# Performance work log

Hardware: AMD Instinct MI355X
Metric: run time of the kernel (lower is better)

## Reference

```python
import jax, jax.numpy as jnp
import numpy as np

B, S, ENC = 64, 60, 1024
E, H, V, T = 512, 512, 32000, 20


def setup_inputs() -> dict:
    key = jax.random.key(0)
    ks = jax.random.split(key, 10)
    sc = lambda n: 1.0 / np.sqrt(n)
    return {
        "encoder_outputs": jax.random.normal(ks[0], (B, S, ENC), jnp.float32),
        "captions": jax.random.randint(ks[1], (B, T), 0, V, jnp.int64),
        "emb_table": jax.random.normal(ks[2], (V, E), jnp.float32) * 0.02,
        "attn_W": jax.random.uniform(ks[3], (H, ENC), jnp.float32, -sc(ENC), sc(ENC)),
        "attn_b": jnp.zeros((H,), jnp.float32),
        "W_ih": jax.random.uniform(ks[4], (4 * H, E + ENC), jnp.float32, -sc(H), sc(H)),
        "W_hh": jax.random.uniform(ks[5], (4 * H, H), jnp.float32, -sc(H), sc(H)),
        "b_ih": jnp.zeros((4 * H,), jnp.float32),
        "b_hh": jnp.zeros((4 * H,), jnp.float32),
        "fc_W": jax.random.uniform(ks[6], (V, H), jnp.float32, -sc(H), sc(H)),
        "fc_b": jnp.zeros((V,), jnp.float32),
    }


def reference(encoder_outputs, captions, emb_table, attn_W, attn_b,
              W_ih, W_hh, b_ih, b_hh, fc_W, fc_b):
    # Luong attention key projection is h-independent: hoist out of the loop.
    proj = jnp.einsum('bse,he->bsh', encoder_outputs, attn_W) + attn_b  # [B,S,H]

    def step(carry, prev_word):
        h, c = carry
        emb = emb_table[prev_word]                                  # [B,E]
        scores = jnp.einsum('bsh,bh->bs', proj, h)                  # [B,S]
        w = jax.nn.softmax(scores, axis=1)
        ctx = jnp.einsum('bs,bse->be', w, encoder_outputs)          # [B,ENC]
        x = jnp.concatenate([emb, ctx], axis=1)                     # [B,E+ENC]
        gates = x @ W_ih.T + b_ih + h @ W_hh.T + b_hh               # [B,4H]
        i, f, g, o = jnp.split(gates, 4, axis=1)
        c2 = jax.nn.sigmoid(f) * c + jax.nn.sigmoid(i) * jnp.tanh(g)
        h2 = jax.nn.sigmoid(o) * jnp.tanh(c2)
        out = h2 @ fc_W.T + fc_b                                    # [B,V] (dropout = eval identity)
        return (h2, c2), (out, w)

    h0 = jnp.zeros((B, H), encoder_outputs.dtype)
    c0 = jnp.zeros((B, H), encoder_outputs.dtype)
    prev_words = captions[:, :-1].T                                 # teacher forcing: [T-1,B]
    _, (outs, attns) = jax.lax.scan(step, (h0, c0), prev_words)
    outputs = jnp.concatenate(
        [jnp.zeros((B, 1, V), outs.dtype), outs.transpose(1, 0, 2)], axis=1)  # [B,T,V]
    return outputs, attns
```

## Files before the change

### kernel.cpp

```cpp
#include <hip/hip_runtime.h>
#include <math.h>
#include <stdint.h>

#define BB   64
#define SS   60
#define ENCD 1024
#define ED   512
#define HD   512
#define VD   32000
#define TT   20

typedef unsigned short u16;
typedef __attribute__((ext_vector_type(8))) short short8v;
typedef __attribute__((ext_vector_type(4))) float f32x4;

__device__ __forceinline__ u16 f2bf(float x) {
  unsigned int u = __float_as_uint(x);
  return (u16)((u + 0x7FFFu + ((u >> 16) & 1u)) >> 16);
}
__device__ __forceinline__ float bf2f(u16 b) {
  return __uint_as_float((unsigned)b << 16);
}

__global__ __launch_bounds__(256) void init_kernel(float* __restrict__ out,
                                                   float* __restrict__ h,
                                                   float* __restrict__ c) {
  int i = blockIdx.x * 256 + threadIdx.x;
  if (i < BB * VD) {
    int b = i / VD, v = i - b * VD;
    out[(long)b * (TT * VD) + v] = 0.f;
  }
  if (i < BB * HD) { h[i] = 0.f; c[i] = 0.f; }
}

__global__ __launch_bounds__(256) void convert_bf16_k(const float* __restrict__ src,
                                                      u16* __restrict__ dst, long n) {
  long i = ((long)blockIdx.x * 256 + threadIdx.x) * 8;
  if (i + 8 <= n) {
    float4 a = *reinterpret_cast<const float4*>(src + i);
    float4 b = *reinterpret_cast<const float4*>(src + i + 4);
    uint4 o;
    o.x = (unsigned)f2bf(a.x) | ((unsigned)f2bf(a.y) << 16);
    o.y = (unsigned)f2bf(a.z) | ((unsigned)f2bf(a.w) << 16);
    o.z = (unsigned)f2bf(b.x) | ((unsigned)f2bf(b.y) << 16);
    o.w = (unsigned)f2bf(b.z) | ((unsigned)f2bf(b.w) << 16);
    *reinterpret_cast<uint4*>(dst + i) = o;
  }
}

__global__ __launch_bounds__(256) void split_pair_k(const float* __restrict__ src,
                                                    u16* __restrict__ bf,
                                                    u16* __restrict__ er, long n) {
  long i = ((long)blockIdx.x * 256 + threadIdx.x) * 8;
  if (i + 8 <= n) {
    #pragma unroll
    for (int j = 0; j < 8; ++j) {
      float v = src[i + j];
      u16 b = f2bf(v);
      bf[i + j] = b;
      er[i + j] = f2bf(v - bf2f(b));
    }
  }
}

__global__ __launch_bounds__(256) void split_wg_k(
    const float* __restrict__ Wih, const float* __restrict__ Whh,
    u16* __restrict__ wb, u16* __restrict__ we) {
  int n = blockIdx.x;
  int k0 = threadIdx.x * 8;
  #pragma unroll
  for (int j = 0; j < 8; ++j) {
    int k = k0 + j;
    float v = (k < 1536) ? Wih[(long)n * 1536 + k] : Whh[(long)n * 512 + (k - 1536)];
    u16 b = f2bf(v);
    wb[(long)n * 2048 + k] = b;
    we[(long)n * 2048 + k] = f2bf(v - bf2f(b));
  }
}

__global__ __launch_bounds__(256) void gather_emb_split(
    const int* __restrict__ caps, const float* __restrict__ emb,
    u16* __restrict__ xb, u16* __restrict__ xe) {
  int r = blockIdx.x;
  int b = r & 63, t = r >> 6;
  int word = caps[b * TT + t];
  const float* src = emb + (long)word * ED;
  for (int k = threadIdx.x; k < ED; k += 256) {
    float v = src[k];
    u16 bb = f2bf(v);
    xb[(long)r * ED + k] = bb;
    xe[(long)r * ED + k] = f2bf(v - bf2f(bb));
  }
}

__global__ __launch_bounds__(256) void gates_mfma(
    const u16* __restrict__ xb, const u16* __restrict__ xe,
    const u16* __restrict__ wb, const u16* __restrict__ we,
    float* __restrict__ P) {
  __shared__ __align__(16) u16 lds[32768];
  const int tid = threadIdx.x;
  const int n0 = blockIdx.x * 64;
  const int kz = blockIdx.z * 256;
  const int w = tid >> 6, lane = tid & 63;
  const int frow = lane & 15, fgrp = lane >> 4;
  const int srow = tid >> 3, sslot = tid & 7;
  const int scol = (sslot ^ (srow & 7)) * 8;
  char* L = (char*)lds;

#define GT_STAGE(buf, kc) do {                                                     \
    _Pragma("unroll")                                                              \
    for (int ii = 0; ii < 2; ++ii) {                                               \
      int r_ = ii * 32 + srow;                                                     \
      __builtin_amdgcn_global_load_lds(                                            \
        (const __attribute__((address_space(1))) void*)(xb + (long)r_ * 2048 + (kc) + scol), \
        (__attribute__((address_space(3))) void*)(L + (buf) * 8192 + ii * 4096 + tid * 16), 16, 0, 0); \
      __builtin_amdgcn_global_load_lds(                                            \
        (const __attribute__((address_space(1))) void*)(xe + (long)r_ * 2048 + (kc) + scol), \
        (__attribute__((address_space(3))) void*)(L + 16384 + (buf) * 8192 + ii * 4096 + tid * 16), 16, 0, 0); \
      __builtin_amdgcn_global_load_lds(                                            \
        (const __attribute__((address_space(1))) void*)(wb + (long)(n0 + r_) * 2048 + (kc) + scol), \
        (__attribute__((address_space(3))) void*)(L + 32768 + (buf) * 8192 + ii * 4096 + tid * 16), 16, 0, 0); \
      __builtin_amdgcn_global_load_lds(                                            \
        (const __attribute__((address_space(1))) void*)(we + (long)(n0 + r_) * 2048 + (kc) + scol), \
        (__attribute__((address_space(3))) void*)(L + 49152 + (buf) * 8192 + ii * 4096 + tid * 16), 16, 0, 0); \
    }                                                                              \
  } while (0)

  f32x4 acc[4] = {{0.f,0.f,0.f,0.f},{0.f,0.f,0.f,0.f},{0.f,0.f,0.f,0.f},{0.f,0.f,0.f,0.f}};

  GT_STAGE(0, kz);
  asm volatile("s_waitcnt vmcnt(0)");
  __syncthreads();

  for (int kc = 0; kc < 4; ++kc) {
    const int cur = kc & 1;
    if (kc < 3) GT_STAGE(cur ^ 1, kz + (kc + 1) * 64);
    const char* Ab = L + cur * 8192;
    const char* Ae = L + 16384 + cur * 8192;
    const char* Bb = L + 32768 + cur * 8192;
    const char* Be = L + 49152 + cur * 8192;
    #pragma unroll
    for (int ks = 0; ks < 2; ++ks) {
      const int slot = ((ks * 4 + fgrp) ^ (frow & 7)) * 16;
      const int brow = (w * 16 + frow) * 128 + slot;
      short8v bbf = *reinterpret_cast<const short8v*>(Bb + brow);
      short8v bef = *reinterpret_cast<const short8v*>(Be + brow);
      #pragma unroll
      for (int m = 0; m < 4; ++m) {
        const int arow = (m * 16 + frow) * 128 + slot;
        short8v abf = *reinterpret_cast<const short8v*>(Ab + arow);
        short8v aef = *reinterpret_cast<const short8v*>(Ae + arow);
        acc[m] = __builtin_amdgcn_mfma_f32_16x16x32_bf16(abf, bbf, acc[m], 0, 0, 0);
        acc[m] = __builtin_amdgcn_mfma_f32_16x16x32_bf16(aef, bbf, acc[m], 0, 0, 0);
        acc[m] = __builtin_amdgcn_mfma_f32_16x16x32_bf16(abf, bef, acc[m], 0, 0, 0);
      }
    }
    asm volatile("s_waitcnt vmcnt(0)");
    __syncthreads();
  }

  float* Pz = P + (long)blockIdx.z * (BB * 2048);
  const int col = n0 + w * 16 + frow;
  #pragma unroll
  for (int m = 0; m < 4; ++m)
    #pragma unroll
    for (int r = 0; r < 4; ++r)
      Pz[(long)(m * 16 + fgrp * 4 + r) * 2048 + col] = acc[m][r];
#undef GT_STAGE
}

__global__ __launch_bounds__(256) void pemb_mfma(
    const u16* __restrict__ xb, const u16* __restrict__ xe,
    const u16* __restrict__ wb, const u16* __restrict__ we,
    float* __restrict__ Pemb) {
  __shared__ __align__(16) u16 lds[32768];
  const int tid = threadIdx.x;
  const int n0 = blockIdx.x * 64;
  const int t  = blockIdx.y;
  const u16* Ab_g = xb + (long)t * 64 * ED;
  const u16* Ae_g = xe + (long)t * 64 * ED;
  const int w = tid >> 6, lane = tid & 63;
  const int frow = lane & 15, fgrp = lane >> 4;
  const int srow = tid >> 3, sslot = tid & 7;
  const int scol = (sslot ^ (srow & 7)) * 8;
  char* L = (char*)lds;

#define PE_STAGE(buf, kc) do {                                                     \
    _Pragma("unroll")                                                              \
    for (int ii = 0; ii < 2; ++ii) {                                               \
      int r_ = ii * 32 + srow;                                                     \
      __builtin_amdgcn_global_load_lds(                                            \
        (const __attribute__((address_space(1))) void*)(Ab_g + (long)r_ * ED + (kc) + scol), \
        (__attribute__((address_space(3))) void*)(L + (buf) * 8192 + ii * 4096 + tid * 16), 16, 0, 0); \
      __builtin_amdgcn_global_load_lds(                                            \
        (const __attribute__((address_space(1))) void*)(Ae_g + (long)r_ * ED + (kc) + scol), \
        (__attribute__((address_space(3))) void*)(L + 16384 + (buf) * 8192 + ii * 4096 + tid * 16), 16, 0, 0); \
      __builtin_amdgcn_global_load_lds(                                            \
        (const __attribute__((address_space(1))) void*)(wb + (long)(n0 + r_) * 2048 + (kc) + scol), \
        (__attribute__((address_space(3))) void*)(L + 32768 + (buf) * 8192 + ii * 4096 + tid * 16), 16, 0, 0); \
      __builtin_amdgcn_global_load_lds(                                            \
        (const __attribute__((address_space(1))) void*)(we + (long)(n0 + r_) * 2048 + (kc) + scol), \
        (__attribute__((address_space(3))) void*)(L + 49152 + (buf) * 8192 + ii * 4096 + tid * 16), 16, 0, 0); \
    }                                                                              \
  } while (0)

  f32x4 acc[4] = {{0.f,0.f,0.f,0.f},{0.f,0.f,0.f,0.f},{0.f,0.f,0.f,0.f},{0.f,0.f,0.f,0.f}};

  PE_STAGE(0, 0);
  asm volatile("s_waitcnt vmcnt(0)");
  __syncthreads();

  for (int kc = 0; kc < 8; ++kc) {
    const int cur = kc & 1;
    if (kc < 7) PE_STAGE(cur ^ 1, (kc + 1) * 64);
    const char* Ab = L + cur * 8192;
    const char* Ae = L + 16384 + cur * 8192;
    const char* Bb = L + 32768 + cur * 8192;
    const char* Be = L + 49152 + cur * 8192;
    #pragma unroll
    for (int ks = 0; ks < 2; ++ks) {
      const int slot = ((ks * 4 + fgrp) ^ (frow & 7)) * 16;
      const int brow = (w * 16 + frow) * 128 + slot;
      short8v bbf = *reinterpret_cast<const short8v*>(Bb + brow);
      short8v bef = *reinterpret_cast<const short8v*>(Be + brow);
      #pragma unroll
      for (int m = 0; m < 4; ++m) {
        const int arow = (m * 16 + frow) * 128 + slot;
        short8v abf = *reinterpret_cast<const short8v*>(Ab + arow);
        short8v aef = *reinterpret_cast<const short8v*>(Ae + arow);
        acc[m] = __builtin_amdgcn_mfma_f32_16x16x32_bf16(abf, bbf, acc[m], 0, 0, 0);
        acc[m] = __builtin_amdgcn_mfma_f32_16x16x32_bf16(aef, bbf, acc[m], 0, 0, 0);
        acc[m] = __builtin_amdgcn_mfma_f32_16x16x32_bf16(abf, bef, acc[m], 0, 0, 0);
      }
    }
    asm volatile("s_waitcnt vmcnt(0)");
    __syncthreads();
  }

  float* Pz = Pemb + (long)t * (BB * 2048);
  const int col = n0 + w * 16 + frow;
  #pragma unroll
  for (int m = 0; m < 4; ++m)
    #pragma unroll
    for (int r = 0; r < 4; ++r)
      Pz[(long)(m * 16 + fgrp * 4 + r) * 2048 + col] = acc[m][r];
#undef PE_STAGE
}

__global__ __launch_bounds__(256) void proj_mfma(
    const u16* __restrict__ eb, const u16* __restrict__ ee,
    const u16* __restrict__ wb, const u16* __restrict__ we,
    const float* __restrict__ bias,
    float* __restrict__ proj) {
  __shared__ __align__(16) u16 lds[32768];
  const int tid = threadIdx.x;
  const int n0 = blockIdx.x * 64;
  const int m0 = blockIdx.y * 64;
  const int w = tid >> 6, lane = tid & 63;
  const int frow = lane & 15, fgrp = lane >> 4;
  const int srow = tid >> 3, sslot = tid & 7;
  const int scol = (sslot ^ (srow & 7)) * 8;
  char* L = (char*)lds;

#define PJ_STAGE(buf, kc) do {                                                     \
    _Pragma("unroll")                                                              \
    for (int ii = 0; ii < 2; ++ii) {                                               \
      int r_ = ii * 32 + srow;                                                     \
      __builtin_amdgcn_global_load_lds(                                            \
        (const __attribute__((address_space(1))) void*)(eb + (long)(m0 + r_) * ENCD + (kc) + scol), \
        (__attribute__((address_space(3))) void*)(L + (buf) * 8192 + ii * 4096 + tid * 16), 16, 0, 0); \
      __builtin_amdgcn_global_load_lds(                                            \
        (const __attribute__((address_space(1))) void*)(ee + (long)(m0 + r_) * ENCD + (kc) + scol), \
        (__attribute__((address_space(3))) void*)(L + 16384 + (buf) * 8192 + ii * 4096 + tid * 16), 16, 0, 0); \
      __builtin_amdgcn_global_load_lds(                                            \
        (const __attribute__((address_space(1))) void*)(wb + (long)(n0 + r_) * ENCD + (kc) + scol), \
        (__attribute__((address_space(3))) void*)(L + 32768 + (buf) * 8192 + ii * 4096 + tid * 16), 16, 0, 0); \
      __builtin_amdgcn_global_load_lds(                                            \
        (const __attribute__((address_space(1))) void*)(we + (long)(n0 + r_) * ENCD + (kc) + scol), \
        (__attribute__((address_space(3))) void*)(L + 49152 + (buf) * 8192 + ii * 4096 + tid * 16), 16, 0, 0); \
    }                                                                              \
  } while (0)

  f32x4 acc[4] = {{0.f,0.f,0.f,0.f},{0.f,0.f,0.f,0.f},{0.f,0.f,0.f,0.f},{0.f,0.f,0.f,0.f}};

  PJ_STAGE(0, 0);
  asm volatile("s_waitcnt vmcnt(0)");
  __syncthreads();

  for (int kc = 0; kc < 16; ++kc) {
    const int cur = kc & 1;
    if (kc < 15) PJ_STAGE(cur ^ 1, (kc + 1) * 64);
    const char* Ab = L + cur * 8192;
    const char* Ae = L + 16384 + cur * 8192;
    const char* Bb = L + 32768 + cur * 8192;
    const char* Be = L + 49152 + cur * 8192;
    #pragma unroll
    for (int ks = 0; ks < 2; ++ks) {
      const int slot = ((ks * 4 + fgrp) ^ (frow & 7)) * 16;
      const int brow = (w * 16 + frow) * 128 + slot;
      short8v bbf = *reinterpret_cast<const short8v*>(Bb + brow);
      short8v bef = *reinterpret_cast<const short8v*>(Be + brow);
      #pragma unroll
      for (int m = 0; m < 4; ++m) {
        const int arow = (m * 16 + frow) * 128 + slot;
        short8v abf = *reinterpret_cast<const short8v*>(Ab + arow);
        short8v aef = *reinterpret_cast<const short8v*>(Ae + arow);
        acc[m] = __builtin_amdgcn_mfma_f32_16x16x32_bf16(abf, bbf, acc[m], 0, 0, 0);
        acc[m] = __builtin_amdgcn_mfma_f32_16x16x32_bf16(aef, bbf, acc[m], 0, 0, 0);
        acc[m] = __builtin_amdgcn_mfma_f32_16x16x32_bf16(abf, bef, acc[m], 0, 0, 0);
      }
    }
    asm volatile("s_waitcnt vmcnt(0)");
    __syncthreads();
  }

  const int col = n0 + w * 16 + frow;
  const float bv = bias[col];
  #pragma unroll
  for (int m = 0; m < 4; ++m)
    #pragma unroll
    for (int r = 0; r < 4; ++r)
      proj[(long)(m0 + m * 16 + fgrp * 4 + r) * HD + col] = acc[m][r] + bv;
#undef PJ_STAGE
}

__global__ __launch_bounds__(256) void fc_tiled(
    const u16* __restrict__ hbuf, const u16* __restrict__ Wb,
    const float* __restrict__ bias, float* __restrict__ out) {
  __shared__ __align__(16) u16 lds[40960];
  const int tid = threadIdx.x;
  const int bid = blockIdx.x;
  const int xcd = bid & 7, loc = bid >> 3;
  const int wg = (xcd < 7) ? (xcd * 297 + loc) : (2079 + loc);
  const int n_tile = wg / 19, t = wg - n_tile * 19;
  const int n0 = n_tile * 256;

  const u16* Ab = hbuf + (long)t * (BB * HD);
  const u16* Wbase = Wb + (long)n0 * HD;

  const int w = tid >> 6, lane = tid & 63;
  const int frow = lane & 15, fgrp = lane >> 4;
  const int srow = tid >> 3, sslot = tid & 7;
  const int scol = (sslot ^ (srow & 7)) * 8;
  char* ldsb = (char*)lds;

#define FC_STAGE(buf, kc) do {                                                    \
    _Pragma("unroll")                                                             \
    for (int ii = 0; ii < 2; ++ii) {                                              \
      __builtin_amdgcn_global_load_lds(                                           \
        (const __attribute__((address_space(1))) void*)(Ab + (ii * 32 + srow) * HD + (kc) + scol), \
        (__attribute__((address_space(3))) void*)(ldsb + (buf) * 8192 + ii * 4096 + tid * 16), \
        16, 0, 0);                                                                \
    }                                                                             \
    _Pragma("unroll")                                                             \
    for (int ii = 0; ii < 8; ++ii) {                                              \
      __builtin_amdgcn_global_load_lds(                                           \
        (const __attribute__((address_space(1))) void*)(Wbase + (long)(ii * 32 + srow) * HD + (kc) + scol), \
        (__attribute__((address_space(3))) void*)(ldsb + 16384 + (buf) * 32768 + ii * 4096 + tid * 16), \
        16, 0, 0);                                                                \
    }                                                                             \
  } while (0)

  f32x4 acc[4][4] = {};

  FC_STAGE(0, 0);
  asm volatile("s_waitcnt vmcnt(0)");
  __syncthreads();

  for (int kc = 0; kc < 8; ++kc) {
    const int cur = kc & 1;
    if (kc < 7) FC_STAGE(cur ^ 1, (kc + 1) * 64);
    const char* Abuf = ldsb + cur * 8192;
    const char* Wbuf = ldsb + 16384 + cur * 32768;
    #pragma unroll
    for (int ks = 0; ks < 2; ++ks) {
      const int slot = ((ks * 4 + fgrp) ^ (frow & 7)) * 16;
      short8v af[4], wf[4];
      #pragma unroll
      for (int m = 0; m < 4; ++m)
        af[m] = *reinterpret_cast<const short8v*>(Abuf + (m * 16 + frow) * 128 + slot);
      #pragma unroll
      for (int n = 0; n < 4; ++n)
        wf[n] = *reinterpret_cast<const short8v*>(Wbuf + (w * 64 + n * 16 + frow) * 128 + slot);
      #pragma unroll
      for (int m = 0; m < 4; ++m)
        #pragma unroll
        for (int n = 0; n < 4; ++n)
          acc[m][n] = __builtin_amdgcn_mfma_f32_16x16x32_bf16(af[m], wf[n], acc[m][n], 0, 0, 0);
    }
    asm volatile("s_waitcnt vmcnt(0)");
    __syncthreads();
  }

  float* Lt = (float*)lds;
  #pragma unroll
  for (int n = 0; n < 4; ++n)
    #pragma unroll
    for (int m = 0; m < 4; ++m)
      #pragma unroll
      for (int r = 0; r < 4; ++r)
        Lt[(m * 16 + fgrp * 4 + r) * 260 + w * 64 + n * 16 + frow] = acc[m][n][r];
  __syncthreads();
  float4 bv4 = *reinterpret_cast<const float4*>(bias + n0 + lane * 4);
  #pragma unroll
  for (int i = 0; i < 16; ++i) {
    int row = w * 16 + i;
    float4 v = *reinterpret_cast<const float4*>(&Lt[row * 260 + lane * 4]);
    v.x += bv4.x; v.y += bv4.y; v.z += bv4.z; v.w += bv4.w;
    *reinterpret_cast<float4*>(out + ((long)row * TT + (t + 1)) * VD + n0 + lane * 4) = v;
  }
#undef FC_STAGE
}

__global__ __launch_bounds__(512) void fused_attn_lstm2(
    const float* __restrict__ proj, const float* __restrict__ enc,
    int t,
    const float* __restrict__ P,
    const float* __restrict__ Pemb_prev,
    const float* __restrict__ b_ih, const float* __restrict__ b_hh,
    const float* __restrict__ c_in, float* __restrict__ c_out,
    u16* __restrict__ hbuf_prev,
    float* __restrict__ attn_out,
    u16* __restrict__ xs_bf, u16* __restrict__ xs_er) {
  int b = blockIdx.x, seg = blockIdx.y;
  __shared__ float sh[HD];
  __shared__ float sc[64];
  __shared__ float sw[64];
  int tid = threadIdx.x;
  if (t > 0) {
    int u = tid;
    const float* pe = Pemb_prev + (long)b * 2048;
    float gi = b_ih[u]        + b_hh[u]        + pe[u];
    float gf = b_ih[u + 512]  + b_hh[u + 512]  + pe[u + 512];
    float gg = b_ih[u + 1024] + b_hh[u + 1024] + pe[u + 1024];
    float go = b_ih[u + 1536] + b_hh[u + 1536] + pe[u + 1536];
    #pragma unroll
    for (int ks = 0; ks < 6; ++ks) {
      const float* p = P + ((long)ks * BB + b) * 2048;
      gi += p[u]; gf += p[u + 512]; gg += p[u + 1024]; go += p[u + 1536];
    }
    float si = 1.f / (1.f + __expf(-gi));
    float sf = 1.f / (1.f + __expf(-gf));
    float so = 1.f / (1.f + __expf(-go));
    float tg = tanhf(gg);
    float c2 = sf * c_in[b * HD + u] + si * tg;
    float h2 = so * tanhf(c2);
    sh[u] = h2;
    if (seg == 0) {
      c_out[b * HD + u] = c2;
      u16 hb16 = f2bf(h2);
      hbuf_prev[b * HD + u] = hb16;
      xs_bf[(long)b * 2048 + 1536 + u] = hb16;
      xs_er[(long)b * 2048 + 1536 + u] = f2bf(h2 - bf2f(hb16));
    }
  } else {
    sh[tid] = 0.f;
    if (seg == 0) {
      xs_bf[(long)b * 2048 + 1536 + tid] = 0;
      xs_er[(long)b * 2048 + 1536 + tid] = 0;
    }
  }
  __syncthreads();
  int wave = tid >> 6, lane = tid & 63;
  for (int s = wave; s < SS; s += 8) {
    const float* pr = proj + ((long)b * SS + s) * HD;
    float acc = 0.f;
    #pragma unroll
    for (int k = 0; k < HD / 64; ++k) acc += pr[lane + k * 64] * sh[lane + k * 64];
    #pragma unroll
    for (int off = 32; off; off >>= 1) acc += __shfl_down(acc, off);
    if (lane == 0) sc[s] = acc;
  }
  __syncthreads();
  if (wave == 0) {
    float v = (lane < SS) ? sc[lane] : -INFINITY;
    float m = v;
    #pragma unroll
    for (int off = 32; off; off >>= 1) m = fmaxf(m, __shfl_down(m, off));
    m = __shfl(m, 0);
    float e = (lane < SS) ? __expf(v - m) : 0.f;
    float sum = e;
    #pragma unroll
    for (int off = 32; off; off >>= 1) sum += __shfl_down(sum, off);
    sum = __shfl(sum, 0);
    float wv = e / sum;
    if (lane < SS) {
      sw[lane] = wv;
      if (seg == 0) attn_out[b * SS + lane] = wv;
    }
  }
  __syncthreads();
  if (tid < 256) {
    int e0 = (seg << 8) + tid;
    float acc = 0.f;
    const float* ebp = enc + (long)b * SS * ENCD + e0;
    #pragma unroll
    for (int s = 0; s < SS; ++s) acc += sw[s] * ebp[(long)s * ENCD];
    u16 bb = f2bf(acc);
    xs_bf[(long)b * 2048 + 512 + e0] = bb;
    xs_er[(long)b * 2048 + 512 + e0] = f2bf(acc - bf2f(bb));
  }
}

__global__ __launch_bounds__(256) void lstm_final2(
    const float* __restrict__ P, const float* __restrict__ Pemb18,
    const float* __restrict__ b_ih, const float* __restrict__ b_hh,
    const float* __restrict__ c_in, u16* __restrict__ hb) {
  int idx = blockIdx.x * 256 + threadIdx.x;
  int b = idx >> 9, u = idx & 511;
  const float* pe = Pemb18 + (long)b * 2048;
  float gi = b_ih[u]        + b_hh[u]        + pe[u];
  float gf = b_ih[u + 512]  + b_hh[u + 512]  + pe[u + 512];
  float gg = b_ih[u + 1024] + b_hh[u + 1024] + pe[u + 1024];
  float go = b_ih[u + 1536] + b_hh[u + 1536] + pe[u + 1536];
  #pragma unroll
  for (int ks = 0; ks < 6; ++ks) {
    const float* p = P + ((long)ks * BB + b) * 2048;
    gi += p[u]; gf += p[u + 512]; gg += p[u + 1024]; go += p[u + 1536];
  }
  float si = 1.f / (1.f + __expf(-gi));
  float sf = 1.f / (1.f + __expf(-gf));
  float so = 1.f / (1.f + __expf(-go));
  float tg = tanhf(gg);
  float c2 = sf * c_in[idx] + si * tg;
  float h2 = so * tanhf(c2);
  hb[idx] = f2bf(h2);
}

extern "C" void kernel_launch(void* const* d_in, const int* in_sizes, int n_in,
                              void* d_out_, int out_size, void* d_ws, size_t ws_size,
                              hipStream_t stream) {
  const float* enc   = (const float*)d_in[0];
  const int*   caps  = (const int*)d_in[1];
  const float* emb   = (const float*)d_in[2];
  const float* attnW = (const float*)d_in[3];
  const float* attnB = (const float*)d_in[4];
  const float* W_ih  = (const float*)d_in[5];
  const float* W_hh  = (const float*)d_in[6];
  const float* b_ih  = (const float*)d_in[7];
  const float* b_hh  = (const float*)d_in[8];
  const float* fcW   = (const float*)d_in[9];
  const float* fcb   = (const float*)d_in[10];

  float* out   = (float*)d_out_;
  float* attns = out + (long)BB * TT * VD;

  float* ws    = (float*)d_ws;
  float* proj  = ws;
  float* h     = proj + (long)BB * SS * HD;
  float* c     = h + BB * HD;
  float* x     = c + BB * HD;
  float* P     = x + BB * 2048;
  u16*   hbuf  = (u16*)(P + (long)8 * BB * 2048);
  u16*   Wbf   = hbuf + (long)(TT - 1) * BB * HD;
  u16*   xs_bf = Wbf + (long)VD * HD;
  u16*   xs_er = xs_bf + (long)BB * 2048;
  u16*   Wg_bf = xs_er + (long)BB * 2048;
  u16*   Wg_er = Wg_bf + (long)2048 * 2048;
  u16*   enc_bf = Wg_er + (long)2048 * 2048;
  u16*   enc_er = enc_bf + (long)BB * SS * ENCD;
  u16*   aW_bf  = enc_er + (long)BB * SS * ENCD;
  u16*   aW_er  = aW_bf + (long)HD * ENCD;
  uintptr_t p9 = (uintptr_t)(aW_er + (long)HD * ENCD);
  p9 = (p9 + 15) & ~(uintptr_t)15;
  float* cbuf1   = (float*)p9;
  u16*   xemb_bf = (u16*)(cbuf1 + BB * HD);
  u16*   xemb_er = xemb_bf + (long)(TT - 1) * BB * ED;
  uintptr_t pA = (uintptr_t)(xemb_er + (long)(TT - 1) * BB * ED);
  pA = (pA + 15) & ~(uintptr_t)15;
  float* Pemb = (float*)pA;

  init_kernel<<<(BB * VD + 255) / 256, 256, 0, stream>>>(out, h, c);

  {
    long n = (long)VD * HD;
    convert_bf16_k<<<(int)(n / 2048), 256, 0, stream>>>(fcW, Wbf, n);
  }
  split_wg_k<<<2048, 256, 0, stream>>>(W_ih, W_hh, Wg_bf, Wg_er);
  {
    long ne = (long)BB * SS * ENCD;
    split_pair_k<<<(int)(ne / 2048), 256, 0, stream>>>(enc, enc_bf, enc_er, ne);
    long nw = (long)HD * ENCD;
    split_pair_k<<<(int)(nw / 2048), 256, 0, stream>>>(attnW, aW_bf, aW_er, nw);
    proj_mfma<<<dim3(8, 60), 256, 0, stream>>>(enc_bf, enc_er, aW_bf, aW_er,
                                               attnB, proj);
  }
  gather_emb_split<<<(TT - 1) * BB, 256, 0, stream>>>(caps, emb, xemb_bf, xemb_er);
  pemb_mfma<<<dim3(32, TT - 1), 256, 0, stream>>>(xemb_bf, xemb_er, Wg_bf, Wg_er,
                                                  Pemb);

  for (int t = 0; t < TT - 1; ++t) {
    const float* c_in = ((t - 1) & 1) ? cbuf1 : c;
    float* c_out = (t & 1) ? cbuf1 : c;
    u16* hbp = hbuf + (long)(t > 0 ? t - 1 : 0) * BB * HD;
    fused_attn_lstm2<<<dim3(BB, 4), 512, 0, stream>>>(
        proj, enc, t, P,
        Pemb + (long)(t > 0 ? t - 1 : 0) * BB * 2048,
        b_ih, b_hh, c_in, c_out, hbp,
        attns + (long)t * BB * SS, xs_bf, xs_er);
    gates_mfma<<<dim3(32, 1, 6), 256, 0, stream>>>(
        xs_bf + 512, xs_er + 512, Wg_bf + 512, Wg_er + 512, P);
  }
  lstm_final2<<<128, 256, 0, stream>>>(P, Pemb + (long)18 * BB * 2048,
                                       b_ih, b_hh, c,
                                       hbuf + (long)(TT - 2) * BB * HD);

  fc_tiled<<<125 * 19, 256, 0, stream>>>(hbuf, Wbf, fcb, out);
}
```

Before: 457.7 us.

## Fuse per-step FC output projection into gates kernel to overlap with recurrence

The vocabulary projection for the previous step's hidden state now runs inside the per-step gates kernel as extra blocks (z>=6), so the FC work fills otherwise idle CUs during the latency-bound recurrence instead of running as one large kernel at the end. Only the last step's FC remains after the loop, in a new 512-thread kernel. This removes the separate large FC launch but makes each per-step launch heavier and could lengthen the critical path if FC blocks compete with the gates blocks.

```diff
diff --git a/kernel.cpp b/kernel.cpp
--- a/kernel.cpp
+++ b/kernel.cpp
@@ -93,19 +93,26 @@
   }
 }
 
-__global__ __launch_bounds__(256) void gates_mfma(
+__global__ __launch_bounds__(256) void gates_fc_mfma(
     const u16* __restrict__ xb, const u16* __restrict__ xe,
     const u16* __restrict__ wb, const u16* __restrict__ we,
-    float* __restrict__ P) {
-  __shared__ __align__(16) u16 lds[32768];
+    float* __restrict__ P,
+    const u16* __restrict__ hb_fc,
+    const u16* __restrict__ Wfc,
+    const float* __restrict__ fcb,
+    float* __restrict__ out_fc,
+    int fc_on) {
+  __shared__ __align__(16) u16 lds[40960];
   const int tid = threadIdx.x;
-  const int n0 = blockIdx.x * 64;
-  const int kz = blockIdx.z * 256;
   const int w = tid >> 6, lane = tid & 63;
   const int frow = lane & 15, fgrp = lane >> 4;
   const int srow = tid >> 3, sslot = tid & 7;
   const int scol = (sslot ^ (srow & 7)) * 8;
-  char* L = (char*)lds;
+
+  if (blockIdx.z < 6) {
+    const int n0 = blockIdx.x * 64;
+    const int kz = blockIdx.z * 256;
+    char* L = (char*)lds;
 
 #define GT_STAGE(buf, kc) do {                                                     \
     _Pragma("unroll")                                                              \
@@ -126,223 +133,55 @@
     }                                                                              \
   } while (0)
 
-  f32x4 acc[4] = {{0.f,0.f,0.f,0.f},{0.f,0.f,0.f,0.f},{0.f,0.f,0.f,0.f},{0.f,0.f,0.f,0.f}};
-
-  GT_STAGE(0, kz);
-  asm volatile("s_waitcnt vmcnt(0)");
-  __syncthreads();
-
-  for (int kc = 0; kc < 4; ++kc) {
-    const int cur = kc & 1;
-    if (kc < 3) GT_STAGE(cur ^ 1, kz + (kc + 1) * 64);
-    const char* Ab = L + cur * 8192;
-    const char* Ae = L + 16384 + cur * 8192;
-    const char* Bb = L + 32768 + cur * 8192;
-    const char* Be = L + 49152 + cur * 8192;
-    #pragma unroll
-    for (int ks = 0; ks < 2; ++ks) {
-      const int slot = ((ks * 4 + fgrp) ^ (frow & 7)) * 16;
-      const int brow = (w * 16 + frow) * 128 + slot;
-      short8v bbf = *reinterpret_cast<const short8v*>(Bb + brow);
-      short8v bef = *reinterpret_cast<const short8v*>(Be + brow);
-      #pragma unroll
-      for (int m = 0; m < 4; ++m) {
-        const int arow = (m * 16 + frow) * 128 + slot;
-        short8v abf = *reinterpret_cast<const short8v*>(Ab + arow);
-        short8v aef = *reinterpret_cast<const short8v*>(Ae + arow);
-        acc[m] = __builtin_amdgcn_mfma_f32_16x16x32_bf16(abf, bbf, acc[m], 0, 0, 0);
-        acc[m] = __builtin_amdgcn_mfma_f32_16x16x32_bf16(aef, bbf, acc[m], 0, 0, 0);
-        acc[m] = __builtin_amdgcn_mfma_f32_16x16x32_bf16(abf, bef, acc[m], 0, 0, 0);
-      }
-    }
+    f32x4 acc[4] = {{0.f,0.f,0.f,0.f},{0.f,0.f,0.f,0.f},{0.f,0.f,0.f,0.f},{0.f,0.f,0.f,0.f}};
+
+    GT_STAGE(0, kz);
     asm volatile("s_waitcnt vmcnt(0)");
     __syncthreads();
-  }
-
-  float* Pz = P + (long)blockIdx.z * (BB * 2048);
-  const int col = n0 + w * 16 + frow;
-  #pragma unroll
-  for (int m = 0; m < 4; ++m)
-    #pragma unroll
-    for (int r = 0; r < 4; ++r)
-      Pz[(long)(m * 16 + fgrp * 4 + r) * 2048 + col] = acc[m][r];
+
+    for (int kc = 0; kc < 4; ++kc) {
+      const int cur = kc & 1;
+      if (kc < 3) GT_STAGE(cur ^ 1, kz + (kc + 1) * 64);
+      const char* Ab = L + cur * 8192;
+      const char* Ae = L + 16384 + cur * 8192;
+      const char* Bb = L + 32768 + cur * 8192;
+      const char* Be = L + 49152 + cur * 8192;
+      #pragma unroll
+      for (int ks = 0; ks < 2; ++ks) {
+        const int slot = ((ks * 4 + fgrp) ^ (frow & 7)) * 16;
+        const int brow = (w * 16 + frow) * 128 + slot;
+        short8v bbf = *reinterpret_cast<const short8v*>(Bb + brow);
+        short8v bef = *reinterpret_cast<const short8v*>(Be + brow);
+        #pragma unroll
+        for (int m = 0; m < 4; ++m) {
+          const int arow = (m * 16 + frow) * 128 + slot;
+          short8v abf = *reinterpret_cast<const short8v*>(Ab + arow);
+          short8v aef = *reinterpret_cast<const short8v*>(Ae + arow);
+          acc[m] = __builtin_amdgcn_mfma_f32_16x16x32_bf16(abf, bbf, acc[m], 0, 0, 0);
+          acc[m] = __builtin_amdgcn_mfma_f32_16x16x32_bf16(aef, bbf, acc[m], 0, 0, 0);
+          acc[m] = __builtin_amdgcn_mfma_f32_16x16x32_bf16(abf, bef, acc[m], 0, 0, 0);
+        }
+      }
+      asm volatile("s_waitcnt vmcnt(0)");
+      __syncthreads();
+    }
+
+    float* Pz = P + (long)blockIdx.z * (BB * 2048);
+    const int col = n0 + w * 16 + frow;
+    #pragma unroll
+    for (int m = 0; m < 4; ++m)
+      #pragma unroll
+      for (int r = 0; r < 4; ++r)
+        Pz[(long)(m * 16 + fgrp * 4 + r) * 2048 + col] = acc[m][r];
 #undef GT_STAGE
-}
-
-__global__ __launch_bounds__(256) void pemb_mfma(
-    const u16* __restrict__ xb, const u16* __restrict__ xe,
-    const u16* __restrict__ wb, const u16* __restrict__ we,
-    float* __restrict__ Pemb) {
-  __shared__ __align__(16) u16 lds[32768];
-  const int tid = threadIdx.x;
-  const int n0 = blockIdx.x * 64;
-  const int t  = blockIdx.y;
-  const u16* Ab_g = xb + (long)t * 64 * ED;
-  const u16* Ae_g = xe + (long)t * 64 * ED;
-  const int w = tid >> 6, lane = tid & 63;
-  const int frow = lane & 15, fgrp = lane >> 4;
-  const int srow = tid >> 3, sslot = tid & 7;
-  const int scol = (sslot ^ (srow & 7)) * 8;
-  char* L = (char*)lds;
-
-#define PE_STAGE(buf, kc) do {                                                     \
-    _Pragma("unroll")                                                              \
-    for (int ii = 0; ii < 2; ++ii) {                                               \
-      int r_ = ii * 32 + srow;                                                     \
-      __builtin_amdgcn_global_load_lds(                                            \
-        (const __attribute__((address_space(1))) void*)(Ab_g + (long)r_ * ED + (kc) + scol), \
-        (__attribute__((address_space(3))) void*)(L + (buf) * 8192 + ii * 4096 + tid * 16), 16, 0, 0); \
-      __builtin_amdgcn_global_load_lds(                                            \
-        (const __attribute__((address_space(1))) void*)(Ae_g + (long)r_ * ED + (kc) + scol), \
-        (__attribute__((address_space(3))) void*)(L + 16384 + (buf) * 8192 + ii * 4096 + tid * 16), 16, 0, 0); \
-      __builtin_amdgcn_global_load_lds(                                            \
-        (const __attribute__((address_space(1))) void*)(wb + (long)(n0 + r_) * 2048 + (kc) + scol), \
-        (__attribute__((address_space(3))) void*)(L + 32768 + (buf) * 8192 + ii * 4096 + tid * 16), 16, 0, 0); \
-      __builtin_amdgcn_global_load_lds(                                            \
-        (const __attribute__((address_space(1))) void*)(we + (long)(n0 + r_) * 2048 + (kc) + scol), \
-        (__attribute__((address_space(3))) void*)(L + 49152 + (buf) * 8192 + ii * 4096 + tid * 16), 16, 0, 0); \
-    }                                                                              \
-  } while (0)
-
-  f32x4 acc[4] = {{0.f,0.f,0.f,0.f},{0.f,0.f,0.f,0.f},{0.f,0.f,0.f,0.f},{0.f,0.f,0.f,0.f}};
-
-  PE_STAGE(0, 0);
-  asm volatile("s_waitcnt vmcnt(0)");
-  __syncthreads();
-
-  for (int kc = 0; kc < 8; ++kc) {
-    const int cur = kc & 1;
-    if (kc < 7) PE_STAGE(cur ^ 1, (kc + 1) * 64);
-    const char* Ab = L + cur * 8192;
-    const char* Ae = L + 16384 + cur * 8192;
-    const char* Bb = L + 32768 + cur * 8192;
-    const char* Be = L + 49152 + cur * 8192;
-    #pragma unroll
-    for (int ks = 0; ks < 2; ++ks) {
-      const int slot = ((ks * 4 + fgrp) ^ (frow & 7)) * 16;
-      const int brow = (w * 16 + frow) * 128 + slot;
-      short8v bbf = *reinterpret_cast<const short8v*>(Bb + brow);
-      short8v bef = *reinterpret_cast<const short8v*>(Be + brow);
-      #pragma unroll
-      for (int m = 0; m < 4; ++m) {
-        const int arow = (m * 16 + frow) * 128 + slot;
-        short8v abf = *reinterpret_cast<const short8v*>(Ab + arow);
-        short8v aef = *reinterpret_cast<const short8v*>(Ae + arow);
-        acc[m] = __builtin_amdgcn_mfma_f32_16x16x32_bf16(abf, bbf, acc[m], 0, 0, 0);
-        acc[m] = __builtin_amdgcn_mfma_f32_16x16x32_bf16(aef, bbf, acc[m], 0, 0, 0);
-        acc[m] = __builtin_amdgcn_mfma_f32_16x16x32_bf16(abf, bef, acc[m], 0, 0, 0);
-      }
-    }
-    asm volatile("s_waitcnt vmcnt(0)");
-    __syncthreads();
-  }
-
-  float* Pz = Pemb + (long)t * (BB * 2048);
-  const int col = n0 + w * 16 + frow;
-  #pragma unroll
-  for (int m = 0; m < 4; ++m)
-    #pragma unroll
-    for (int r = 0; r < 4; ++r)
-      Pz[(long)(m * 16 + fgrp * 4 + r) * 2048 + col] = acc[m][r];
-#undef PE_STAGE
-}
-
-__global__ __launch_bounds__(256) void proj_mfma(
-    const u16* __restrict__ eb, const u16* __restrict__ ee,
-    const u16* __restrict__ wb, const u16* __restrict__ we,
-    const float* __restrict__ bias,
-    float* __restrict__ proj) {
-  __shared__ __align__(16) u16 lds[32768];
-  const int tid = threadIdx.x;
-  const int n0 = blockIdx.x * 64;
-  const int m0 = blockIdx.y * 64;
-  const int w = tid >> 6, lane = tid & 63;
-  const int frow = lane & 15, fgrp = lane >> 4;
-  const int srow = tid >> 3, sslot = tid & 7;
-  const int scol = (sslot ^ (srow & 7)) * 8;
-  char* L = (char*)lds;
-
-#define PJ_STAGE(buf, kc) do {                                                     \
-    _Pragma("unroll")                                                              \
-    for (int ii = 0; ii < 2; ++ii) {                                               \
-      int r_ = ii * 32 + srow;                                                     \
-      __builtin_amdgcn_global_load_lds(                                            \
-        (const __attribute__((address_space(1))) void*)(eb + (long)(m0 + r_) * ENCD + (kc) + scol), \
-        (__attribute__((address_space(3))) void*)(L + (buf) * 8192 + ii * 4096 + tid * 16), 16, 0, 0); \
-      __builtin_amdgcn_global_load_lds(                                            \
-        (const __attribute__((address_space(1))) void*)(ee + (long)(m0 + r_) * ENCD + (kc) + scol), \
-        (__attribute__((address_space(3))) void*)(L + 16384 + (buf) * 8192 + ii * 4096 + tid * 16), 16, 0, 0); \
-      __builtin_amdgcn_global_load_lds(                                            \
-        (const __attribute__((address_space(1))) void*)(wb + (long)(n0 + r_) * ENCD + (kc) + scol), \
-        (__attribute__((address_space(3))) void*)(L + 32768 + (buf) * 8192 + ii * 4096 + tid * 16), 16, 0, 0); \
-      __builtin_amdgcn_global_load_lds(                                            \
-        (const __attribute__((address_space(1))) void*)(we + (long)(n0 + r_) * ENCD + (kc) + scol), \
-        (__attribute__((address_space(3))) void*)(L + 49152 + (buf) * 8192 + ii * 4096 + tid * 16), 16, 0, 0); \
-    }                                                                              \
-  } while (0)
-
-  f32x4 acc[4] = {{0.f,0.f,0.f,0.f},{0.f,0.f,0.f,0.f},{0.f,0.f,0.f,0.f},{0.f,0.f,0.f,0.f}};
-
-  PJ_STAGE(0, 0);
-  asm volatile("s_waitcnt vmcnt(0)");
-  __syncthreads();
-
-  for (int kc = 0; kc < 16; ++kc) {
-    const int cur = kc & 1;
-    if (kc < 15) PJ_STAGE(cur ^ 1, (kc + 1) * 64);
-    const char* Ab = L + cur * 8192;
-    const char* Ae = L + 16384 + cur * 8192;
-    const char* Bb = L + 32768 + cur * 8192;
-    const char* Be = L + 49152 + cur * 8192;
-    #pragma unroll
-    for (int ks = 0; ks < 2; ++ks) {
-      const int slot = ((ks * 4 + fgrp) ^ (frow & 7)) * 16;
-      const int brow = (w * 16 + frow) * 128 + slot;
-      short8v bbf = *reinterpret_cast<const short8v*>(Bb + brow);
-      short8v bef = *reinterpret_cast<const short8v*>(Be + brow);
-      #pragma unroll
-      for (int m = 0; m < 4; ++m) {
-        const int arow = (m * 16 + frow) * 128 + slot;
-        short8v abf = *reinterpret_cast<const short8v*>(Ab + arow);
-        short8v aef = *reinterpret_cast<const short8v*>(Ae + arow);
-        acc[m] = __builtin_amdgcn_mfma_f32_16x16x32_bf16(abf, bbf, acc[m], 0, 0, 0);
-        acc[m] = __builtin_amdgcn_mfma_f32_16x16x32_bf16(aef, bbf, acc[m], 0, 0, 0);
-        acc[m] = __builtin_amdgcn_mfma_f32_16x16x32_bf16(abf, bef, acc[m], 0, 0, 0);
-      }
-    }
-    asm volatile("s_waitcnt vmcnt(0)");
-    __syncthreads();
-  }
-
-  const int col = n0 + w * 16 + frow;
-  const float bv = bias[col];
-  #pragma unroll
-  for (int m = 0; m < 4; ++m)
-    #pragma unroll
-    for (int r = 0; r < 4; ++r)
-      proj[(long)(m0 + m * 16 + fgrp * 4 + r) * HD + col] = acc[m][r] + bv;
-#undef PJ_STAGE
-}
-
-__global__ __launch_bounds__(256) void fc_tiled(
-    const u16* __restrict__ hbuf, const u16* __restrict__ Wb,
-    const float* __restrict__ bias, float* __restrict__ out) {
-  __shared__ __align__(16) u16 lds[40960];
-  const int tid = threadIdx.x;
-  const int bid = blockIdx.x;
-  const int xcd = bid & 7, loc = bid >> 3;
-  const int wg = (xcd < 7) ? (xcd * 297 + loc) : (2079 + loc);
-  const int n_tile = wg / 19, t = wg - n_tile * 19;
-  const int n0 = n_tile * 256;
-
-  const u16* Ab = hbuf + (long)t * (BB * HD);
-  const u16* Wbase = Wb + (long)n0 * HD;
-
-  const int w = tid >> 6, lane = tid & 63;
-  const int frow = lane & 15, fgrp = lane >> 4;
-  const int srow = tid >> 3, sslot = tid & 7;
-  const int scol = (sslot ^ (srow & 7)) * 8;
-  char* ldsb = (char*)lds;
+  } else {
+    if (!fc_on) return;
+    const int nt = (blockIdx.z - 6) * 32 + blockIdx.x;
+    if (nt >= 125) return;
+    const int n0 = nt * 256;
+    const u16* Ab = hb_fc;
+    const u16* Wbase = Wfc + (long)n0 * HD;
+    char* ldsb = (char*)lds;
 
 #define FC_STAGE(buf, kc) do {                                                    \
     _Pragma("unroll")                                                             \
@@ -361,31 +200,270 @@
     }                                                                             \
   } while (0)
 
-  f32x4 acc[4][4] = {};
-
-  FC_STAGE(0, 0);
+    f32x4 acc[4][4] = {};
+
+    FC_STAGE(0, 0);
+    asm volatile("s_waitcnt vmcnt(0)");
+    __syncthreads();
+
+    for (int kc = 0; kc < 8; ++kc) {
+      const int cur = kc & 1;
+      if (kc < 7) FC_STAGE(cur ^ 1, (kc + 1) * 64);
+      const char* Abuf = ldsb + cur * 8192;
+      const char* Wbuf = ldsb + 16384 + cur * 32768;
+      #pragma unroll
+      for (int ks = 0; ks < 2; ++ks) {
+        const int slot = ((ks * 4 + fgrp) ^ (frow & 7)) * 16;
+        short8v af[4], wf[4];
+        #pragma unroll
+        for (int m = 0; m < 4; ++m)
+          af[m] = *reinterpret_cast<const short8v*>(Abuf + (m * 16 + frow) * 128 + slot);
+        #pragma unroll
+        for (int n = 0; n < 4; ++n)
+          wf[n] = *reinterpret_cast<const short8v*>(Wbuf + (w * 64 + n * 16 + frow) * 128 + slot);
+        #pragma unroll
+        for (int m = 0; m < 4; ++m)
+          #pragma unroll
+          for (int n = 0; n < 4; ++n)
+            acc[m][n] = __builtin_amdgcn_mfma_f32_16x16x32_bf16(af[m], wf[n], acc[m][n], 0, 0, 0);
+      }
+      asm volatile("s_waitcnt vmcnt(0)");
+      __syncthreads();
+    }
+
+    float* Lt = (float*)lds;
+    #pragma unroll
+    for (int n = 0; n < 4; ++n)
+      #pragma unroll
+      for (int m = 0; m < 4; ++m)
+        #pragma unroll
+        for (int r = 0; r < 4; ++r)
+          Lt[(m * 16 + fgrp * 4 + r) * 260 + w * 64 + n * 16 + frow] = acc[m][n][r];
+    __syncthreads();
+    float4 bv4 = *reinterpret_cast<const float4*>(fcb + n0 + lane * 4);
+    #pragma unroll
+    for (int i = 0; i < 16; ++i) {
+      int row = w * 16 + i;
+      float4 v = *reinterpret_cast<const float4*>(&Lt[row * 260 + lane * 4]);
+      v.x += bv4.x; v.y += bv4.y; v.z += bv4.z; v.w += bv4.w;
+      *reinterpret_cast<float4*>(out_fc + (long)row * ((long)TT * VD) + n0 + lane * 4) = v;
+    }
+#undef FC_STAGE
+  }
+}
+
+__global__ __launch_bounds__(256) void pemb_mfma(
+    const u16* __restrict__ xb, const u16* __restrict__ xe,
+    const u16* __restrict__ wb, const u16* __restrict__ we,
+    float* __restrict__ Pemb) {
+  __shared__ __align__(16) u16 lds[32768];
+  const int tid = threadIdx.x;
+  const int n0 = blockIdx.x * 64;
+  const int t  = blockIdx.y;
+  const u16* Ab_g = xb + (long)t * 64 * ED;
+  const u16* Ae_g = xe + (long)t * 64 * ED;
+  const int w = tid >> 6, lane = tid & 63;
+  const int frow = lane & 15, fgrp = lane >> 4;
+  const int srow = tid >> 3, sslot = tid & 7;
+  const int scol = (sslot ^ (srow & 7)) * 8;
+  char* L = (char*)lds;
+
+#define PE_STAGE(buf, kc) do {                                                     \
+    _Pragma("unroll")                                                              \
+    for (int ii = 0; ii < 2; ++ii) {                                               \
+      int r_ = ii * 32 + srow;                                                     \
+      __builtin_amdgcn_global_load_lds(                                            \
+        (const __attribute__((address_space(1))) void*)(Ab_g + (long)r_ * ED + (kc) + scol), \
+        (__attribute__((address_space(3))) void*)(L + (buf) * 8192 + ii * 4096 + tid * 16), 16, 0, 0); \
+      __builtin_amdgcn_global_load_lds(                                            \
+        (const __attribute__((address_space(1))) void*)(Ae_g + (long)r_ * ED + (kc) + scol), \
+        (__attribute__((address_space(3))) void*)(L + 16384 + (buf) * 8192 + ii * 4096 + tid * 16), 16, 0, 0); \
+      __builtin_amdgcn_global_load_lds(                                            \
+        (const __attribute__((address_space(1))) void*)(wb + (long)(n0 + r_) * 2048 + (kc) + scol), \
+        (__attribute__((address_space(3))) void*)(L + 32768 + (buf) * 8192 + ii * 4096 + tid * 16), 16, 0, 0); \
+      __builtin_amdgcn_global_load_lds(                                            \
+        (const __attribute__((address_space(1))) void*)(we + (long)(n0 + r_) * 2048 + (kc) + scol), \
+        (__attribute__((address_space(3))) void*)(L + 49152 + (buf) * 8192 + ii * 4096 + tid * 16), 16, 0, 0); \
+    }                                                                              \
+  } while (0)
+
+  f32x4 acc[4] = {{0.f,0.f,0.f,0.f},{0.f,0.f,0.f,0.f},{0.f,0.f,0.f,0.f},{0.f,0.f,0.f,0.f}};
+
+  PE_STAGE(0, 0);
   asm volatile("s_waitcnt vmcnt(0)");
   __syncthreads();
 
   for (int kc = 0; kc < 8; ++kc) {
     const int cur = kc & 1;
-    if (kc < 7) FC_STAGE(cur ^ 1, (kc + 1) * 64);
+    if (kc < 7) PE_STAGE(cur ^ 1, (kc + 1) * 64);
+    const char* Ab = L + cur * 8192;
+    const char* Ae = L + 16384 + cur * 8192;
+    const char* Bb = L + 32768 + cur * 8192;
+    const char* Be = L + 49152 + cur * 8192;
+    #pragma unroll
+    for (int ks = 0; ks < 2; ++ks) {
+      const int slot = ((ks * 4 + fgrp) ^ (frow & 7)) * 16;
+      const int brow = (w * 16 + frow) * 128 + slot;
+      short8v bbf = *reinterpret_cast<const short8v*>(Bb + brow);
+      short8v bef = *reinterpret_cast<const short8v*>(Be + brow);
+      #pragma unroll
+      for (int m = 0; m < 4; ++m) {
+        const int arow = (m * 16 + frow) * 128 + slot;
+        short8v abf = *reinterpret_cast<const short8v*>(Ab + arow);
+        short8v aef = *reinterpret_cast<const short8v*>(Ae + arow);
+        acc[m] = __builtin_amdgcn_mfma_f32_16x16x32_bf16(abf, bbf, acc[m], 0, 0, 0);
+        acc[m] = __builtin_amdgcn_mfma_f32_16x16x32_bf16(aef, bbf, acc[m], 0, 0, 0);
+        acc[m] = __builtin_amdgcn_mfma_f32_16x16x32_bf16(abf, bef, acc[m], 0, 0, 0);
+      }
+    }
+    asm volatile("s_waitcnt vmcnt(0)");
+    __syncthreads();
+  }
+
+  float* Pz = Pemb + (long)t * (BB * 2048);
+  const int col = n0 + w * 16 + frow;
+  #pragma unroll
+  for (int m = 0; m < 4; ++m)
+    #pragma unroll
+    for (int r = 0; r < 4; ++r)
+      Pz[(long)(m * 16 + fgrp * 4 + r) * 2048 + col] = acc[m][r];
+#undef PE_STAGE
+}
+
+__global__ __launch_bounds__(256) void proj_mfma(
+    const u16* __restrict__ eb, const u16* __restrict__ ee,
+    const u16* __restrict__ wb, const u16* __restrict__ we,
+    const float* __restrict__ bias,
+    float* __restrict__ proj) {
+  __shared__ __align__(16) u16 lds[32768];
+  const int tid = threadIdx.x;
+  const int n0 = blockIdx.x * 64;
+  const int m0 = blockIdx.y * 64;
+  const int w = tid >> 6, lane = tid & 63;
+  const int frow = lane & 15, fgrp = lane >> 4;
+  const int srow = tid >> 3, sslot = tid & 7;
+  const int scol = (sslot ^ (srow & 7)) * 8;
+  char* L = (char*)lds;
+
+#define PJ_STAGE(buf, kc) do {                                                     \
+    _Pragma("unroll")                                                              \
+    for (int ii = 0; ii < 2; ++ii) {                                               \
+      int r_ = ii * 32 + srow;                                                     \
+      __builtin_amdgcn_global_load_lds(                                            \
+        (const __attribute__((address_space(1))) void*)(eb + (long)(m0 + r_) * ENCD + (kc) + scol), \
+        (__attribute__((address_space(3))) void*)(L + (buf) * 8192 + ii * 4096 + tid * 16), 16, 0, 0); \
+      __builtin_amdgcn_global_load_lds(                                            \
+        (const __attribute__((address_space(1))) void*)(ee + (long)(m0 + r_) * ENCD + (kc) + scol), \
+        (__attribute__((address_space(3))) void*)(L + 16384 + (buf) * 8192 + ii * 4096 + tid * 16), 16, 0, 0); \
+      __builtin_amdgcn_global_load_lds(                                            \
+        (const __attribute__((address_space(1))) void*)(wb + (long)(n0 + r_) * ENCD + (kc) + scol), \
+        (__attribute__((address_space(3))) void*)(L + 32768 + (buf) * 8192 + ii * 4096 + tid * 16), 16, 0, 0); \
+      __builtin_amdgcn_global_load_lds(                                            \
+        (const __attribute__((address_space(1))) void*)(we + (long)(n0 + r_) * ENCD + (kc) + scol), \
+        (__attribute__((address_space(3))) void*)(L + 49152 + (buf) * 8192 + ii * 4096 + tid * 16), 16, 0, 0); \
+    }                                                                              \
+  } while (0)
+
+  f32x4 acc[4] = {{0.f,0.f,0.f,0.f},{0.f,0.f,0.f,0.f},{0.f,0.f,0.f,0.f},{0.f,0.f,0.f,0.f}};
+
+  PJ_STAGE(0, 0);
+  asm volatile("s_waitcnt vmcnt(0)");
+  __syncthreads();
+
+  for (int kc = 0; kc < 16; ++kc) {
+    const int cur = kc & 1;
+    if (kc < 15) PJ_STAGE(cur ^ 1, (kc + 1) * 64);
+    const char* Ab = L + cur * 8192;
+    const char* Ae = L + 16384 + cur * 8192;
+    const char* Bb = L + 32768 + cur * 8192;
+    const char* Be = L + 49152 + cur * 8192;
+    #pragma unroll
+    for (int ks = 0; ks < 2; ++ks) {
+      const int slot = ((ks * 4 + fgrp) ^ (frow & 7)) * 16;
+      const int brow = (w * 16 + frow) * 128 + slot;
+      short8v bbf = *reinterpret_cast<const short8v*>(Bb + brow);
+      short8v bef = *reinterpret_cast<const short8v*>(Be + brow);
+      #pragma unroll
+      for (int m = 0; m < 4; ++m) {
+        const int arow = (m * 16 + frow) * 128 + slot;
+        short8v abf = *reinterpret_cast<const short8v*>(Ab + arow);
+        short8v aef = *reinterpret_cast<const short8v*>(Ae + arow);
+        acc[m] = __builtin_amdgcn_mfma_f32_16x16x32_bf16(abf, bbf, acc[m], 0, 0, 0);
+        acc[m] = __builtin_amdgcn_mfma_f32_16x16x32_bf16(aef, bbf, acc[m], 0, 0, 0);
+        acc[m] = __builtin_amdgcn_mfma_f32_16x16x32_bf16(abf, bef, acc[m], 0, 0, 0);
+      }
+    }
+    asm volatile("s_waitcnt vmcnt(0)");
+    __syncthreads();
+  }
+
+  const int col = n0 + w * 16 + frow;
+  const float bv = bias[col];
+  #pragma unroll
+  for (int m = 0; m < 4; ++m)
+    #pragma unroll
+    for (int r = 0; r < 4; ++r)
+      proj[(long)(m0 + m * 16 + fgrp * 4 + r) * HD + col] = acc[m][r] + bv;
+#undef PJ_STAGE
+}
+
+__global__ __launch_bounds__(512) void fc_last(
+    const u16* __restrict__ hb,
+    const u16* __restrict__ Wb,
+    const float* __restrict__ bias,
+    float* __restrict__ outp) {
+  __shared__ __align__(16) u16 lds[40960];
+  const int tid = threadIdx.x;
+  const int n0 = blockIdx.x * 256;
+
+  const u16* Ab = hb;
+  const u16* Wbase = Wb + (long)n0 * HD;
+
+  const int w = tid >> 6, lane = tid & 63;
+  const int frow = lane & 15, fgrp = lane >> 4;
+  const int srow = tid >> 3, sslot = tid & 7;
+  const int scol = (sslot ^ (srow & 7)) * 8;
+  char* ldsb = (char*)lds;
+
+#define FL_STAGE(buf, kc) do {                                                    \
+    __builtin_amdgcn_global_load_lds(                                             \
+        (const __attribute__((address_space(1))) void*)(Ab + srow * HD + (kc) + scol), \
+        (__attribute__((address_space(3))) void*)(ldsb + (buf) * 8192 + tid * 16),    \
+        16, 0, 0);                                                                \
+    _Pragma("unroll")                                                             \
+    for (int ii = 0; ii < 4; ++ii) {                                              \
+      __builtin_amdgcn_global_load_lds(                                           \
+        (const __attribute__((address_space(1))) void*)(Wbase + (long)(ii * 64 + srow) * HD + (kc) + scol), \
+        (__attribute__((address_space(3))) void*)(ldsb + 16384 + (buf) * 32768 + ii * 8192 + tid * 16), \
+        16, 0, 0);                                                                \
+    }                                                                             \
+  } while (0)
+
+  f32x4 acc[4][2] = {};
+
+  FL_STAGE(0, 0);
+  asm volatile("s_waitcnt vmcnt(0)");
+  __syncthreads();
+
+  for (int kc = 0; kc < 8; ++kc) {
+    const int cur = kc & 1;
+    if (kc < 7) FL_STAGE(cur ^ 1, (kc + 1) * 64);
     const char* Abuf = ldsb + cur * 8192;
     const char* Wbuf = ldsb + 16384 + cur * 32768;
     #pragma unroll
     for (int ks = 0; ks < 2; ++ks) {
       const int slot = ((ks * 4 + fgrp) ^ (frow & 7)) * 16;
-      short8v af[4], wf[4];
+      short8v af[4], wf[2];
       #pragma unroll
       for (int m = 0; m < 4; ++m)
         af[m] = *reinterpret_cast<const short8v*>(Abuf + (m * 16 + frow) * 128 + slot);
       #pragma unroll
-      for (int n = 0; n < 4; ++n)
-        wf[n] = *reinterpret_cast<const short8v*>(Wbuf + (w * 64 + n * 16 + frow) * 128 + slot);
+      for (int n = 0; n < 2; ++n)
+        wf[n] = *reinterpret_cast<const short8v*>(Wbuf + (w * 32 + n * 16 + frow) * 128 + slot);
       #pragma unroll
       for (int m = 0; m < 4; ++m)
         #pragma unroll
-        for (int n = 0; n < 4; ++n)
+        for (int n = 0; n < 2; ++n)
           acc[m][n] = __builtin_amdgcn_mfma_f32_16x16x32_bf16(af[m], wf[n], acc[m][n], 0, 0, 0);
     }
     asm volatile("s_waitcnt vmcnt(0)");
@@ -394,22 +472,22 @@
 
   float* Lt = (float*)lds;
   #pragma unroll
-  for (int n = 0; n < 4; ++n)
+  for (int n = 0; n < 2; ++n)
     #pragma unroll
     for (int m = 0; m < 4; ++m)
       #pragma unroll
       for (int r = 0; r < 4; ++r)
-        Lt[(m * 16 + fgrp * 4 + r) * 260 + w * 64 + n * 16 + frow] = acc[m][n][r];
+        Lt[(m * 16 + fgrp * 4 + r) * 260 + w * 32 + n * 16 + frow] = acc[m][n][r];
   __syncthreads();
   float4 bv4 = *reinterpret_cast<const float4*>(bias + n0 + lane * 4);
   #pragma unroll
-  for (int i = 0; i < 16; ++i) {
-    int row = w * 16 + i;
+  for (int i = 0; i < 8; ++i) {
+    int row = i * 8 + w;
     float4 v = *reinterpret_cast<const float4*>(&Lt[row * 260 + lane * 4]);
     v.x += bv4.x; v.y += bv4.y; v.z += bv4.z; v.w += bv4.w;
-    *reinterpret_cast<float4*>(out + ((long)row * TT + (t + 1)) * VD + n0 + lane * 4) = v;
-  }
-#undef FC_STAGE
+    *reinterpret_cast<float4*>(outp + (long)row * ((long)TT * VD) + n0 + lane * 4) = v;
+  }
+#undef FL_STAGE
 }
 
 __global__ __launch_bounds__(512) void fused_attn_lstm2(
@@ -598,12 +676,14 @@
         Pemb + (long)(t > 0 ? t - 1 : 0) * BB * 2048,
         b_ih, b_hh, c_in, c_out, hbp,
         attns + (long)t * BB * SS, xs_bf, xs_er);
-    gates_mfma<<<dim3(32, 1, 6), 256, 0, stream>>>(
-        xs_bf + 512, xs_er + 512, Wg_bf + 512, Wg_er + 512, P);
+    gates_fc_mfma<<<dim3(32, 1, 10), 256, 0, stream>>>(
+        xs_bf + 512, xs_er + 512, Wg_bf + 512, Wg_er + 512, P,
+        hbp, Wbf, fcb, out + (long)t * VD, t > 0 ? 1 : 0);
   }
   lstm_final2<<<128, 256, 0, stream>>>(P, Pemb + (long)18 * BB * 2048,
                                        b_ih, b_hh, c,
                                        hbuf + (long)(TT - 2) * BB * HD);
 
-  fc_tiled<<<125 * 19, 256, 0, stream>>>(hbuf, Wbf, fcb, out);
-}
+  fc_last<<<125, 512, 0, stream>>>(hbuf + (long)18 * BB * HD, Wbf, fcb,
+                                   out + (long)19 * VD);
+}
```

Result: slower. 519.3 us (+13.4%).
